# Kernel tuning notes

Measured on AMD Instinct MI355X. Metric: run time of the kernel, lower is better.

## Reference

```python
import jax, jax.numpy as jnp
import numpy as np

D_MODEL = 256
D_INNER = 512      # expand(2) * d_model
D_STATE = 16
DT_RANK = 16       # ceil(256/16)
D_CONV = 4
DEPTH = 2


def _silu(x):
    return x * jax.nn.sigmoid(x)


def _selective_scan(u, dt, A, B, C, D):
    # u,dt: [b,l,d]; A: [d,n]; B,C: [b,l,n]; D: [d]
    dA = jnp.einsum('bld,dn->bldn', dt, A)
    dBu = jnp.einsum('bld,bld,bln->bldn', dt, u, B)
    # torch: F.pad(dA[:,1:], last-l-dim one zero).flip(1).cumsum(1).exp().flip(1)
    dA_shift = jnp.concatenate([dA[:, 1:], jnp.zeros_like(dA[:, :1])], axis=1)
    dAc = jnp.exp(jnp.cumsum(dA_shift[:, ::-1], axis=1)[:, ::-1])
    x = jnp.cumsum(dBu * dAc, axis=1) / (dAc + 1e-12)
    y = jnp.einsum('bldn,bln->bld', x, C)
    return y + u * D


def _block(x, p):
    # x: [b,l,d_model]
    in_w, conv_w, conv_b, xproj_w, dt_w, dt_b, A_log, Dp, out_w = p
    xr = jnp.einsum('bld,ed->ble', x, in_w)           # [b,l,2*d_inner]
    xx, res = jnp.split(xr, 2, axis=-1)
    # causal depthwise conv1d (padding d_conv-1 then truncate == left-pad)
    xc = jax.lax.conv_general_dilated(
        xx.transpose(0, 2, 1), conv_w, window_strides=(1,),
        padding=[(D_CONV - 1, 0)], feature_group_count=D_INNER,
        dimension_numbers=('NCH', 'OIH', 'NCH')) + conv_b[None, :, None]
    xx = _silu(xc.transpose(0, 2, 1))                 # [b,l,d_inner]
    x_dbl = jnp.einsum('bld,ed->ble', xx, xproj_w)
    delta = x_dbl[..., :DT_RANK]
    B = x_dbl[..., DT_RANK:DT_RANK + D_STATE]
    C = x_dbl[..., DT_RANK + D_STATE:]
    delta = jax.nn.softplus(jnp.einsum('blr,dr->bld', delta, dt_w) + dt_b)
    A = -jnp.exp(A_log)
    y = _selective_scan(xx, delta, A, B, C, Dp)
    y = y * _silu(res)
    return jnp.einsum('bld,od->blo', y, out_w)


def _model1(x, params):
    for i in range(DEPTH):
        x = _block(x, tuple(q[i] for q in params))
    return x


def setup_inputs() -> dict:
    key = jax.random.key(0)
    ks = jax.random.split(key, 8)

    def nrm(k, shape, scale):
        return (jax.random.normal(k, shape) * scale).astype(jnp.float32)

    x0 = jax.random.normal(ks[0], (4, D_MODEL, 256, 256), jnp.float32)
    in_w = nrm(ks[1], (DEPTH, 2 * D_INNER, D_MODEL), 0.02)
    conv_w = nrm(ks[2], (DEPTH, D_INNER, 1, D_CONV), 0.1)
    conv_b = jnp.zeros((DEPTH, D_INNER), jnp.float32)
    xproj_w = nrm(ks[3], (DEPTH, DT_RANK + 2 * D_STATE, D_INNER), 0.02)
    dt_w = nrm(ks[4], (DEPTH, D_INNER, DT_RANK), 0.05)
    dt_b = jnp.full((DEPTH, D_INNER), -4.0, jnp.float32)  # small deltas for stability
    A_log = jnp.tile(jnp.log(jnp.arange(1, D_STATE + 1, dtype=jnp.float32))[None, None, :],
                     (DEPTH, D_INNER, 1))
    Dp = jnp.ones((DEPTH, D_INNER), jnp.float32)
    out_w = nrm(ks[5], (DEPTH, D_MODEL, D_INNER), 0.02)
    return dict(x0=x0, in_w=in_w, conv_w=conv_w, conv_b=conv_b, xproj_w=xproj_w,
                dt_w=dt_w, dt_b=dt_b, A_log=A_log, Dp=Dp, out_w=out_w)


def reference(x0, in_w, conv_w, conv_b, xproj_w, dt_w, dt_b, A_log, Dp, out_w):
    params = (in_w, conv_w, conv_b, xproj_w, dt_w, dt_b, A_log, Dp, out_w)
    # h-axis: pool over w, mamba over length h (weights shared with w pass)
    x_h = x0.mean(axis=3)                                        # [b,c,h]
    xm_h = _model1(x_h.transpose(0, 2, 1), params)               # [b,h,c]
    xm_h = xm_h.transpose(0, 2, 1)[..., None] * x0               # [b,c,h,w]
    # w-axis: pool over h of gated map, mamba over length w
    x_w = xm_h.mean(axis=2)                                      # [b,c,w]
    xm_w = _model1(x_w.transpose(0, 2, 1), params)               # [b,w,c]
    return xm_w.transpose(0, 2, 1)[:, :, None, :] * x0           # [b,c,h,w]
```

## Files before the change

### kernel.cpp

```cpp
#include <hip/hip_runtime.h>
#include <math.h>

#define BSZ 4
#define DM 256
#define LL 256
#define DI 512
#define NBL (BSZ * LL)

__device__ __forceinline__ float fast_rcp(float x) { return __builtin_amdgcn_rcpf(x); }
__device__ __forceinline__ float fast_sig(float x) { return fast_rcp(1.0f + __expf(-x)); }

__device__ __forceinline__ void unswz(int j, int& b, int& i) {
    b = (j & 7) >> 1;
    i = ((j >> 3) << 1) | (j & 1);
}

__global__ __launch_bounds__(256) void k_meanw_prep(const float* __restrict__ x0,
                                                    const float* __restrict__ in_w1,
                                                    const float* __restrict__ out_w0,
                                                    float* __restrict__ S0,
                                                    float* __restrict__ Wf) {
    __shared__ float smem[1664];
    int bl = blockIdx.x;
    int tid = threadIdx.x;
    if (bl < 1024) {
        int b, i; unswz(bl, b, i);
        int rowblk = (b << 8) | i;
        int wv = tid >> 6, lane = tid & 63;
        const float4* x4 = (const float4*)x0;
        int rbase = rowblk * 256 + wv * 64;
        for (int i0 = 0; i0 < 64; i0 += 8) {
            float s[8];
#pragma unroll
            for (int j = 0; j < 8; ++j) {
                float4 v = x4[(size_t)(rbase + i0 + j) * 64 + lane];
                s[j] = (v.x + v.y) + (v.z + v.w);
            }
#pragma unroll
            for (int j = 0; j < 8; ++j) {
#pragma unroll
                for (int m = 32; m >= 1; m >>= 1) s[j] += __shfl_xor(s[j], m);
            }
            if (lane == 0) {
#pragma unroll
                for (int j = 0; j < 8; ++j) {
                    int rr = rbase + i0 + j;
                    int bb = rr >> 16, d = (rr >> 8) & 255, h = rr & 255;
                    S0[((size_t)(bb * LL) + h) * DM + d] = s[j] * (1.0f / 256.0f);
                }
            }
        }
    } else {
        float* As = smem;
        float* Bs = smem + 576;
        int t = bl - 1024;
        int e0 = (t >> 4) * 32, k0c = (t & 15) * 32;
        int tx = tid & 15, ty = tid >> 4;
        float acc00 = 0.f, acc01 = 0.f, acc10 = 0.f, acc11 = 0.f;
        for (int dm0 = 0; dm0 < 256; dm0 += 16) {
            float4 v;
            if (tid < 128) {
                int r = tid >> 2, q = tid & 3;
                v = *(const float4*)(in_w1 + (size_t)(e0 + r) * 256 + dm0 + 4 * q);
            } else {
                int idx = tid - 128;
                int r = idx >> 3, q = idx & 7;
                v = *(const float4*)(out_w0 + (size_t)(dm0 + r) * 512 + k0c + 4 * q);
            }
            __syncthreads();
            if (tid < 128) {
                int r = tid >> 2, q = tid & 3;
                As[(4 * q + 0) * 36 + r] = v.x;
                As[(4 * q + 1) * 36 + r] = v.y;
                As[(4 * q + 2) * 36 + r] = v.z;
                As[(4 * q + 3) * 36 + r] = v.w;
            } else {
                int idx = tid - 128;
                int r = idx >> 3, q = idx & 7;
                Bs[r * 36 + 4 * q + 0] = v.x;
                Bs[r * 36 + 4 * q + 1] = v.y;
                Bs[r * 36 + 4 * q + 2] = v.z;
                Bs[r * 36 + 4 * q + 3] = v.w;
            }
            __syncthreads();
#pragma unroll
            for (int kk = 0; kk < 16; ++kk) {
                float2 a = *(const float2*)(As + kk * 36 + 2 * ty);
                float2 b2 = *(const float2*)(Bs + kk * 36 + 2 * tx);
                acc00 = fmaf(a.x, b2.x, acc00);
                acc01 = fmaf(a.x, b2.y, acc01);
                acc10 = fmaf(a.y, b2.x, acc10);
                acc11 = fmaf(a.y, b2.y, acc11);
            }
        }
        float* c0 = Wf + (size_t)(e0 + 2 * ty) * 512 + k0c + 2 * tx;
        c0[0] = acc00; c0[1] = acc01;
        c0[512] = acc10; c0[513] = acc11;
    }
}

__global__ __launch_bounds__(256) void k_gemm_nt64(const float* __restrict__ A,
                                                   const float* __restrict__ Bw,
                                                   float* __restrict__ C) {
    __shared__ float As[16][68];
    __shared__ float Bs[16][68];
    int tid = threadIdx.x;
    int b, i; unswz(blockIdx.x, b, i);
    int m0 = b * 256 + (i >> 4) * 64;
    int n0 = (i & 15) * 64;
    int tx = tid & 15, ty = tid >> 4;
    int r = tid >> 2, kq = (tid & 3) * 4;

    const float* pa = A + (size_t)(m0 + r) * 256 + kq;
    const float* pb = Bw + (size_t)(n0 + r) * 256 + kq;
    float4 ra = *(const float4*)pa;
    float4 rb = *(const float4*)pb;

    float acc[4][4];
#pragma unroll
    for (int ii = 0; ii < 4; ++ii)
#pragma unroll
        for (int jj = 0; jj < 4; ++jj) acc[ii][jj] = 0.0f;

    for (int k0 = 0; k0 < 256; k0 += 16) {
        __syncthreads();
        As[kq + 0][r] = ra.x; As[kq + 1][r] = ra.y; As[kq + 2][r] = ra.z; As[kq + 3][r] = ra.w;
        Bs[kq + 0][r] = rb.x; Bs[kq + 1][r] = rb.y; Bs[kq + 2][r] = rb.z; Bs[kq + 3][r] = rb.w;
        __syncthreads();
        if (k0 + 16 < 256) {
            ra = *(const float4*)(pa + k0 + 16);
            rb = *(const float4*)(pb + k0 + 16);
        }
#pragma unroll
        for (int kk = 0; kk < 16; ++kk) {
            float4 a4 = *(const float4*)(&As[kk][ty * 4]);
            float4 b4 = *(const float4*)(&Bs[kk][tx * 4]);
            float aa[4] = {a4.x, a4.y, a4.z, a4.w};
            float bb[4] = {b4.x, b4.y, b4.z, b4.w};
#pragma unroll
            for (int ii = 0; ii < 4; ++ii)
#pragma unroll
                for (int jj = 0; jj < 4; ++jj)
                    acc[ii][jj] = fmaf(aa[ii], bb[jj], acc[ii][jj]);
        }
    }
#pragma unroll
    for (int ii = 0; ii < 4; ++ii) {
        float4 o;
        o.x = acc[ii][0]; o.y = acc[ii][1]; o.z = acc[ii][2]; o.w = acc[ii][3];
        *(float4*)(C + (size_t)(m0 + ty * 4 + ii) * 1024 + n0 + tx * 4) = o;
    }
}

__global__ __launch_bounds__(256) void k_gemm_tn64(const float* __restrict__ At,
                                                   const float* __restrict__ Bw,
                                                   float* __restrict__ C) {
    __shared__ float As[16][68];
    __shared__ float Bs[16][68];
    int tid = threadIdx.x;
    int b, i; unswz(blockIdx.x, b, i);
    int l0 = (i >> 4) * 64;
    int n0 = (i & 15) * 64;
    int m0 = b * 256 + l0;
    int tx = tid & 15, ty = tid >> 4;
    int rkk = tid >> 4, mq = (tid & 15) * 4;
    int rn = tid >> 2, dq = (tid & 3) * 4;

    const float* pa = At + ((size_t)(b * 512) + rkk) * 256 + l0 + mq;
    const float* pb = Bw + (size_t)(n0 + rn) * 512 + dq;
    float4 ra = *(const float4*)pa;
    float4 rb = *(const float4*)pb;

    float acc[4][4];
#pragma unroll
    for (int ii = 0; ii < 4; ++ii)
#pragma unroll
        for (int jj = 0; jj < 4; ++jj) acc[ii][jj] = 0.0f;

    for (int d0 = 0; d0 < 512; d0 += 16) {
        __syncthreads();
        *(float4*)(&As[rkk][mq]) = ra;
        Bs[dq + 0][rn] = rb.x; Bs[dq + 1][rn] = rb.y; Bs[dq + 2][rn] = rb.z; Bs[dq + 3][rn] = rb.w;
        __syncthreads();
        if (d0 + 16 < 512) {
            ra = *(const float4*)(pa + (size_t)(d0 + 16) * 256);
            rb = *(const float4*)(pb + d0 + 16);
        }
#pragma unroll
        for (int kk = 0; kk < 16; ++kk) {
            float4 a4 = *(const float4*)(&As[kk][ty * 4]);
            float4 b4 = *(const float4*)(&Bs[kk][tx * 4]);
            float aa[4] = {a4.x, a4.y, a4.z, a4.w};
            float bb[4] = {b4.x, b4.y, b4.z, b4.w};
#pragma unroll
            for (int ii = 0; ii < 4; ++ii)
#pragma unroll
                for (int jj = 0; jj < 4; ++jj)
                    acc[ii][jj] = fmaf(aa[ii], bb[jj], acc[ii][jj]);
        }
    }
#pragma unroll
    for (int ii = 0; ii < 4; ++ii) {
        float4 o;
        o.x = acc[ii][0]; o.y = acc[ii][1]; o.z = acc[ii][2]; o.w = acc[ii][3];
        *(float4*)(C + (size_t)(m0 + ty * 4 + ii) * 1024 + n0 + tx * 4) = o;
    }
}

__global__ __launch_bounds__(256) void k_mid(const float* __restrict__ xz,
                                             const float* __restrict__ cw,
                                             const float* __restrict__ cb,
                                             const float* __restrict__ xpw,
                                             float* __restrict__ xx,
                                             float* __restrict__ xdbl) {
    __shared__ float xs[DI];
    __shared__ float pr[256];
    int tid = threadIdx.x;
    int b = (blockIdx.x & 7) >> 1;
    int ib = ((blockIdx.x >> 3) << 1) | (blockIdx.x & 1);

    for (int k = 0; k < 4; ++k) {
        int l = ib + 64 * k;
        int bl = (b << 8) | l;
        __syncthreads();
#pragma unroll
        for (int c = 0; c < 2; ++c) {
            int d = tid + 256 * c;
            float4 w4 = *(const float4*)(cw + d * 4);
            float acc = cb[d];
#pragma unroll
            for (int kk = 0; kk < 4; ++kk) {
                int ls = l + kk - 3;
                float v = (ls >= 0) ? xz[((size_t)(b * LL + ls)) * 1024 + d] : 0.0f;
                acc = fmaf(((const float*)&w4)[kk], v, acc);
            }
            float v = acc * fast_sig(acc);
            xs[d] = v;
            xx[(size_t)bl * DI + d] = v;
        }
        __syncthreads();

        int e = tid >> 2, c2 = tid & 3;
        float a = 0.0f;
        if (e < 48) {
            const float4* xv4 = (const float4*)(xs + c2 * 128);
            const float4* wv4 = (const float4*)(xpw + (size_t)e * DI + c2 * 128);
#pragma unroll 8
            for (int q = 0; q < 32; ++q) {
                float4 x4 = xv4[q], p4 = wv4[q];
                a = fmaf(x4.x, p4.x, a);
                a = fmaf(x4.y, p4.y, a);
                a = fmaf(x4.z, p4.z, a);
                a = fmaf(x4.w, p4.w, a);
            }
        }
        pr[tid] = a;
        __syncthreads();
        if (tid < 48)
            xdbl[(size_t)bl * 48 + tid] = pr[4 * tid] + pr[4 * tid + 1] + pr[4 * tid + 2] + pr[4 * tid + 3];
    }
}

__global__ __launch_bounds__(256) void k_scan(const float* __restrict__ xx,
                                              const float* __restrict__ xdbl,
                                              const float* __restrict__ xz,
                                              const float* __restrict__ Alog,
                                              const float* __restrict__ Dp,
                                              const float* __restrict__ dtw,
                                              const float* __restrict__ dtb,
                                              float* __restrict__ ygT) {
    __shared__ float yred[4][LL];
    __shared__ float us[LL];
    int tid = threadIdx.x;
    int lane = tid & 63, w = tid >> 6;
    int b = (blockIdx.x & 7) >> 1;
    int ib = ((blockIdx.x >> 3) << 1) | (blockIdx.x & 1);
    int l0 = lane * 4;

    for (int kq = 0; kq < 4; ++kq) {
        int d = ib + 128 * kq;
        int seq = b * DI + d;
        __syncthreads();

        const float* xd0 = xdbl + ((size_t)(b * LL) + l0) * 48;
        const float* wr = dtw + d * 16;
        float4 w0 = *(const float4*)(wr + 0);
        float4 w1 = *(const float4*)(wr + 4);
        float4 w2 = *(const float4*)(wr + 8);
        float4 w3 = *(const float4*)(wr + 12);
        float bias = dtb[d];

        float dt[4], u[4], dtu[4], P[4];
#pragma unroll
        for (int i = 0; i < 4; ++i) {
            const float* xr = xd0 + i * 48;
            float4 a0 = *(const float4*)(xr + 0);
            float4 a1 = *(const float4*)(xr + 4);
            float4 a2 = *(const float4*)(xr + 8);
            float4 a3 = *(const float4*)(xr + 12);
            float acc = bias;
            acc = fmaf(a0.x, w0.x, acc); acc = fmaf(a0.y, w0.y, acc);
            acc = fmaf(a0.z, w0.z, acc); acc = fmaf(a0.w, w0.w, acc);
            acc = fmaf(a1.x, w1.x, acc); acc = fmaf(a1.y, w1.y, acc);
            acc = fmaf(a1.z, w1.z, acc); acc = fmaf(a1.w, w1.w, acc);
            acc = fmaf(a2.x, w2.x, acc); acc = fmaf(a2.y, w2.y, acc);
            acc = fmaf(a2.z, w2.z, acc); acc = fmaf(a2.w, w2.w, acc);
            acc = fmaf(a3.x, w3.x, acc); acc = fmaf(a3.y, w3.y, acc);
            acc = fmaf(a3.z, w3.z, acc); acc = fmaf(a3.w, w3.w, acc);
            dt[i] = (acc > 20.0f) ? acc : __logf(1.0f + __expf(acc));
            u[i] = xx[((size_t)(b * LL) + l0 + i) * DI + d];
            dtu[i] = dt[i] * u[i];
        }

        P[0] = dt[0]; P[1] = P[0] + dt[1]; P[2] = P[1] + dt[2]; P[3] = P[2] + dt[3];
        float s = P[3];
#pragma unroll
        for (int off = 1; off < 64; off <<= 1) {
            float t = __shfl_up(s, off);
            if (lane >= off) s += t;
        }
        float base = s - P[3];
        float dt_end = __shfl(s, 63);
        float Dtc[4];
#pragma unroll
        for (int i = 0; i < 4; ++i) Dtc[i] = P[i] + base;

        if (w == 0) {
#pragma unroll
            for (int i = 0; i < 4; ++i) us[l0 + i] = u[i];
        }

        float4 Al = *(const float4*)(Alog + d * 16 + 4 * w);
        float A[4] = {-__expf(Al.x), -__expf(Al.y), -__expf(Al.z), -__expf(Al.w)};
        float Bv[4][4], Cv[4][4];
#pragma unroll
        for (int i = 0; i < 4; ++i) {
            float4 bq = *(const float4*)(xd0 + i * 48 + 16 + 4 * w);
            float4 cq = *(const float4*)(xd0 + i * 48 + 32 + 4 * w);
            Bv[i][0] = bq.x; Bv[i][1] = bq.y; Bv[i][2] = bq.z; Bv[i][3] = bq.w;
            Cv[i][0] = cq.x; Cv[i][1] = cq.y; Cv[i][2] = cq.z; Cv[i][3] = cq.w;
        }

        float y[4] = {0.f, 0.f, 0.f, 0.f};
#pragma unroll
        for (int c = 0; c < 4; ++c) {
            float Ac = A[c];
            float dAc[4], t[4];
#pragma unroll
            for (int i = 0; i < 4; ++i) {
                dAc[i] = __expf(Ac * (dt_end - Dtc[i]));
                t[i] = dtu[i] * Bv[i][c] * dAc[i];
            }
            float p0 = t[0], p1 = p0 + t[1], p2 = p1 + t[2], p3 = p2 + t[3];
            float ss = p3;
#pragma unroll
            for (int off = 1; off < 64; off <<= 1) {
                float tt = __shfl_up(ss, off);
                if (lane >= off) ss += tt;
            }
            float baseT = ss - p3;
            y[0] = fmaf((p0 + baseT) * fast_rcp(dAc[0] + 1e-12f), Cv[0][c], y[0]);
            y[1] = fmaf((p1 + baseT) * fast_rcp(dAc[1] + 1e-12f), Cv[1][c], y[1]);
            y[2] = fmaf((p2 + baseT) * fast_rcp(dAc[2] + 1e-12f), Cv[2][c], y[2]);
            y[3] = fmaf((p3 + baseT) * fast_rcp(dAc[3] + 1e-12f), Cv[3][c], y[3]);
        }
#pragma unroll
        for (int i = 0; i < 4; ++i) yred[w][l0 + i] = y[i];
        __syncthreads();

        int l = tid;
        float ysum = yred[0][l] + yred[1][l] + yred[2][l] + yred[3][l];
        float yv = fmaf(us[l], Dp[d], ysum);
        float res = xz[((size_t)(b * LL) + l) * 1024 + DI + d];
        ygT[(size_t)seq * LL + l] = yv * res * fast_sig(res);
    }
}

__device__ __forceinline__ void outproj_col(const float* __restrict__ ygT,
                                            const float* __restrict__ w1row,
                                            int b, int tid,
                                            float* ws, float* ms) {
    ws[tid] = w1row[tid];
    ws[tid + 256] = w1row[tid + 256];
    __syncthreads();
    const float* yb = ygT + (size_t)(b * 512) * 256 + tid;
    float a0 = 0.f, a1 = 0.f, a2 = 0.f, a3 = 0.f;
#pragma unroll 2
    for (int dd = 0; dd < 512; dd += 8) {
        float v0 = yb[(dd + 0) * 256], v1 = yb[(dd + 1) * 256];
        float v2 = yb[(dd + 2) * 256], v3 = yb[(dd + 3) * 256];
        float v4 = yb[(dd + 4) * 256], v5 = yb[(dd + 5) * 256];
        float v6 = yb[(dd + 6) * 256], v7 = yb[(dd + 7) * 256];
        a0 = fmaf(v0, ws[dd + 0], a0);
        a1 = fmaf(v1, ws[dd + 1], a1);
        a2 = fmaf(v2, ws[dd + 2], a2);
        a3 = fmaf(v3, ws[dd + 3], a3);
        a0 = fmaf(v4, ws[dd + 4], a0);
        a1 = fmaf(v5, ws[dd + 5], a1);
        a2 = fmaf(v6, ws[dd + 6], a2);
        a3 = fmaf(v7, ws[dd + 7], a3);
    }
    ms[tid] = (a0 + a1) + (a2 + a3);
    __syncthreads();
}

__global__ __launch_bounds__(256) void k_outproj_fuse_mean_h(const float* __restrict__ ygT,
                                                             const float* __restrict__ w1,
                                                             const float* __restrict__ x0,
                                                             float* __restrict__ xw) {
    __shared__ float ws[512];
    __shared__ float ms[LL];
    int b, d; unswz(blockIdx.x, b, d);
    int bd = (b << 8) | d;
    int tid = threadIdx.x;
    outproj_col(ygT, w1 + (size_t)d * 512, b, tid, ws, ms);

    int w = tid;
    const float* xrow = x0 + (size_t)bd * 65536;
    float a0 = 0.0f, a1 = 0.0f, a2 = 0.0f, a3 = 0.0f;
    for (int h = 0; h < 256; h += 8) {
        float xv[8];
#pragma unroll
        for (int j = 0; j < 8; ++j) xv[j] = xrow[(size_t)(h + j) * 256 + w];
        a0 = fmaf(ms[h + 0], xv[0], a0);
        a1 = fmaf(ms[h + 1], xv[1], a1);
        a2 = fmaf(ms[h + 2], xv[2], a2);
        a3 = fmaf(ms[h + 3], xv[3], a3);
        a0 = fmaf(ms[h + 4], xv[4], a0);
        a1 = fmaf(ms[h + 5], xv[5], a1);
        a2 = fmaf(ms[h + 6], xv[6], a2);
        a3 = fmaf(ms[h + 7], xv[7], a3);
    }
    float acc = (a0 + a1) + (a2 + a3);
    xw[((size_t)(b * LL) + w) * DM + d] = acc * (1.0f / 256.0f);
}

__global__ __launch_bounds__(256) void k_outproj_final(const float* __restrict__ ygT,
                                                       const float* __restrict__ w1,
                                                       const float* __restrict__ x0,
                                                       float* __restrict__ out) {
    __shared__ float ws[512];
    __shared__ float ms[LL];
    int b, d; unswz(blockIdx.x, b, d);
    int bd = (b << 8) | d;
    int tid = threadIdx.x;
    outproj_col(ygT, w1 + (size_t)d * 512, b, tid, ws, ms);

    int w4 = tid & 63;
    int hq = tid >> 6;
    float4 mv = *(const float4*)(ms + (w4 << 2));
    const float4* xin = (const float4*)(x0 + (size_t)bd * 65536);
    float4* oout = (float4*)(out + (size_t)bd * 65536);
#pragma unroll 4
    for (int hi = 0; hi < 64; ++hi) {
        int h = hi * 4 + hq;
        size_t idx = (size_t)h * 64 + w4;
        float4 xv = xin[idx];
        float4 o;
        o.x = mv.x * xv.x;
        o.y = mv.y * xv.y;
        o.z = mv.z * xv.z;
        o.w = mv.w * xv.w;
        oout[idx] = o;
    }
}

extern "C" void kernel_launch(void* const* d_in, const int* in_sizes, int n_in,
                              void* d_out, int out_size, void* d_ws, size_t ws_size,
                              hipStream_t stream) {
    const float* x0      = (const float*)d_in[0];
    const float* in_w    = (const float*)d_in[1];
    const float* conv_w  = (const float*)d_in[2];
    const float* conv_b  = (const float*)d_in[3];
    const float* xproj_w = (const float*)d_in[4];
    const float* dt_w    = (const float*)d_in[5];
    const float* dt_b    = (const float*)d_in[6];
    const float* A_log   = (const float*)d_in[7];
    const float* Dp      = (const float*)d_in[8];
    const float* out_w   = (const float*)d_in[9];
    float* out = (float*)d_out;

    float* S0   = (float*)d_ws;
    float* Wf   = S0 + 262144;
    float* xz   = Wf + 524288;
    float* xx   = xz + 1048576;
    float* xdbl = xx + 524288;
    float* ygT  = xdbl + 49152;

    const float* out_w1 = out_w + 131072;

    auto run_model_core = [&](const float* inb) {
        k_gemm_nt64<<<256, 256, 0, stream>>>(inb, in_w, xz);
        k_mid<<<256, 256, 0, stream>>>(xz, conv_w, conv_b, xproj_w, xx, xdbl);
        k_scan<<<512, 256, 0, stream>>>(xx, xdbl, xz, A_log, Dp, dt_w, dt_b, ygT);
        k_gemm_tn64<<<256, 256, 0, stream>>>(ygT, Wf, xz);
        k_mid<<<256, 256, 0, stream>>>(xz, conv_w + 2048, conv_b + 512,
                                       xproj_w + 24576, xx, xdbl);
        k_scan<<<512, 256, 0, stream>>>(xx, xdbl, xz, A_log + 8192, Dp + 512,
                                        dt_w + 8192, dt_b + 512, ygT);
    };

    k_meanw_prep<<<1536, 256, 0, stream>>>(x0, in_w + 262144, out_w, S0, Wf);
    run_model_core(S0);
    k_outproj_fuse_mean_h<<<NBL, 256, 0, stream>>>(ygT, out_w1, x0, S0);
    run_model_core(S0);
    k_outproj_final<<<NBL, 256, 0, stream>>>(ygT, out_w1, x0, out);
}
```

Baseline: 472.7 us.

## Store pooled inputs transposed and recompute causal conv in scan

```diff
diff --git a/kernel.cpp b/kernel.cpp
--- a/kernel.cpp
+++ b/kernel.cpp
@@ -18,14 +18,14 @@
 __global__ __launch_bounds__(256) void k_meanw_prep(const float* __restrict__ x0,
                                                     const float* __restrict__ in_w1,
                                                     const float* __restrict__ out_w0,
-                                                    float* __restrict__ S0,
+                                                    float* __restrict__ S0T,
                                                     float* __restrict__ Wf) {
     __shared__ float smem[1664];
     int bl = blockIdx.x;
     int tid = threadIdx.x;
     if (bl < 1024) {
-        int b, i; unswz(bl, b, i);
-        int rowblk = (b << 8) | i;
+        int b, dch; unswz(bl, b, dch);
+        int rowblk = (b << 8) | dch;
         int wv = tid >> 6, lane = tid & 63;
         const float4* x4 = (const float4*)x0;
         int rbase = rowblk * 256 + wv * 64;
@@ -42,12 +42,13 @@
                 for (int m = 32; m >= 1; m >>= 1) s[j] += __shfl_xor(s[j], m);
             }
             if (lane == 0) {
-#pragma unroll
-                for (int j = 0; j < 8; ++j) {
-                    int rr = rbase + i0 + j;
-                    int bb = rr >> 16, d = (rr >> 8) & 255, h = rr & 255;
-                    S0[((size_t)(bb * LL) + h) * DM + d] = s[j] * (1.0f / 256.0f);
-                }
+                float4 o1, o2;
+                o1.x = s[0] * (1.0f / 256.0f); o1.y = s[1] * (1.0f / 256.0f);
+                o1.z = s[2] * (1.0f / 256.0f); o1.w = s[3] * (1.0f / 256.0f);
+                o2.x = s[4] * (1.0f / 256.0f); o2.y = s[5] * (1.0f / 256.0f);
+                o2.z = s[6] * (1.0f / 256.0f); o2.w = s[7] * (1.0f / 256.0f);
+                *(float4*)(S0T + (size_t)rbase + i0) = o1;
+                *(float4*)(S0T + (size_t)rbase + i0 + 4) = o2;
             }
         }
     } else {
@@ -99,62 +100,9 @@
     }
 }
 
-__global__ __launch_bounds__(256) void k_gemm_nt64(const float* __restrict__ A,
-                                                   const float* __restrict__ Bw,
-                                                   float* __restrict__ C) {
-    __shared__ float As[16][68];
-    __shared__ float Bs[16][68];
-    int tid = threadIdx.x;
-    int b, i; unswz(blockIdx.x, b, i);
-    int m0 = b * 256 + (i >> 4) * 64;
-    int n0 = (i & 15) * 64;
-    int tx = tid & 15, ty = tid >> 4;
-    int r = tid >> 2, kq = (tid & 3) * 4;
-
-    const float* pa = A + (size_t)(m0 + r) * 256 + kq;
-    const float* pb = Bw + (size_t)(n0 + r) * 256 + kq;
-    float4 ra = *(const float4*)pa;
-    float4 rb = *(const float4*)pb;
-
-    float acc[4][4];
-#pragma unroll
-    for (int ii = 0; ii < 4; ++ii)
-#pragma unroll
-        for (int jj = 0; jj < 4; ++jj) acc[ii][jj] = 0.0f;
-
-    for (int k0 = 0; k0 < 256; k0 += 16) {
-        __syncthreads();
-        As[kq + 0][r] = ra.x; As[kq + 1][r] = ra.y; As[kq + 2][r] = ra.z; As[kq + 3][r] = ra.w;
-        Bs[kq + 0][r] = rb.x; Bs[kq + 1][r] = rb.y; Bs[kq + 2][r] = rb.z; Bs[kq + 3][r] = rb.w;
-        __syncthreads();
-        if (k0 + 16 < 256) {
-            ra = *(const float4*)(pa + k0 + 16);
-            rb = *(const float4*)(pb + k0 + 16);
-        }
-#pragma unroll
-        for (int kk = 0; kk < 16; ++kk) {
-            float4 a4 = *(const float4*)(&As[kk][ty * 4]);
-            float4 b4 = *(const float4*)(&Bs[kk][tx * 4]);
-            float aa[4] = {a4.x, a4.y, a4.z, a4.w};
-            float bb[4] = {b4.x, b4.y, b4.z, b4.w};
-#pragma unroll
-            for (int ii = 0; ii < 4; ++ii)
-#pragma unroll
-                for (int jj = 0; jj < 4; ++jj)
-                    acc[ii][jj] = fmaf(aa[ii], bb[jj], acc[ii][jj]);
-        }
-    }
-#pragma unroll
-    for (int ii = 0; ii < 4; ++ii) {
-        float4 o;
-        o.x = acc[ii][0]; o.y = acc[ii][1]; o.z = acc[ii][2]; o.w = acc[ii][3];
-        *(float4*)(C + (size_t)(m0 + ty * 4 + ii) * 1024 + n0 + tx * 4) = o;
-    }
-}
-
-__global__ __launch_bounds__(256) void k_gemm_tn64(const float* __restrict__ At,
-                                                   const float* __restrict__ Bw,
-                                                   float* __restrict__ C) {
+__global__ __launch_bounds__(256) void k_gemm_tn_inproj(const float* __restrict__ S0T,
+                                                        const float* __restrict__ Bw,
+                                                        float* __restrict__ C) {
     __shared__ float As[16][68];
     __shared__ float Bs[16][68];
     int tid = threadIdx.x;
@@ -166,8 +114,8 @@
     int rkk = tid >> 4, mq = (tid & 15) * 4;
     int rn = tid >> 2, dq = (tid & 3) * 4;
 
-    const float* pa = At + ((size_t)(b * 512) + rkk) * 256 + l0 + mq;
-    const float* pb = Bw + (size_t)(n0 + rn) * 512 + dq;
+    const float* pa = S0T + ((size_t)(b * 256) + rkk) * 256 + l0 + mq;
+    const float* pb = Bw + (size_t)(n0 + rn) * 256 + dq;
     float4 ra = *(const float4*)pa;
     float4 rb = *(const float4*)pb;
 
@@ -177,12 +125,12 @@
 #pragma unroll
         for (int jj = 0; jj < 4; ++jj) acc[ii][jj] = 0.0f;
 
-    for (int d0 = 0; d0 < 512; d0 += 16) {
+    for (int d0 = 0; d0 < 256; d0 += 16) {
         __syncthreads();
         *(float4*)(&As[rkk][mq]) = ra;
         Bs[dq + 0][rn] = rb.x; Bs[dq + 1][rn] = rb.y; Bs[dq + 2][rn] = rb.z; Bs[dq + 3][rn] = rb.w;
         __syncthreads();
-        if (d0 + 16 < 512) {
+        if (d0 + 16 < 256) {
             ra = *(const float4*)(pa + (size_t)(d0 + 16) * 256);
             rb = *(const float4*)(pb + d0 + 16);
         }
@@ -207,11 +155,65 @@
     }
 }
 
+__global__ __launch_bounds__(256) void k_gemm_tn64(const float* __restrict__ At,
+                                                   const float* __restrict__ Bw,
+                                                   float* __restrict__ C) {
+    __shared__ float As[16][68];
+    __shared__ float Bs[16][68];
+    int tid = threadIdx.x;
+    int b, i; unswz(blockIdx.x, b, i);
+    int l0 = (i >> 4) * 64;
+    int n0 = (i & 15) * 64;
+    int m0 = b * 256 + l0;
+    int tx = tid & 15, ty = tid >> 4;
+    int rkk = tid >> 4, mq = (tid & 15) * 4;
+    int rn = tid >> 2, dq = (tid & 3) * 4;
+
+    const float* pa = At + ((size_t)(b * 512) + rkk) * 256 + l0 + mq;
+    const float* pb = Bw + (size_t)(n0 + rn) * 512 + dq;
+    float4 ra = *(const float4*)pa;
+    float4 rb = *(const float4*)pb;
+
+    float acc[4][4];
+#pragma unroll
+    for (int ii = 0; ii < 4; ++ii)
+#pragma unroll
+        for (int jj = 0; jj < 4; ++jj) acc[ii][jj] = 0.0f;
+
+    for (int d0 = 0; d0 < 512; d0 += 16) {
+        __syncthreads();
+        *(float4*)(&As[rkk][mq]) = ra;
+        Bs[dq + 0][rn] = rb.x; Bs[dq + 1][rn] = rb.y; Bs[dq + 2][rn] = rb.z; Bs[dq + 3][rn] = rb.w;
+        __syncthreads();
+        if (d0 + 16 < 512) {
+            ra = *(const float4*)(pa + (size_t)(d0 + 16) * 256);
+            rb = *(const float4*)(pb + d0 + 16);
+        }
+#pragma unroll
+        for (int kk = 0; kk < 16; ++kk) {
+            float4 a4 = *(const float4*)(&As[kk][ty * 4]);
+            float4 b4 = *(const float4*)(&Bs[kk][tx * 4]);
+            float aa[4] = {a4.x, a4.y, a4.z, a4.w};
+            float bb[4] = {b4.x, b4.y, b4.z, b4.w};
+#pragma unroll
+            for (int ii = 0; ii < 4; ++ii)
+#pragma unroll
+                for (int jj = 0; jj < 4; ++jj)
+                    acc[ii][jj] = fmaf(aa[ii], bb[jj], acc[ii][jj]);
+        }
+    }
+#pragma unroll
+    for (int ii = 0; ii < 4; ++ii) {
+        float4 o;
+        o.x = acc[ii][0]; o.y = acc[ii][1]; o.z = acc[ii][2]; o.w = acc[ii][3];
+        *(float4*)(C + (size_t)(m0 + ty * 4 + ii) * 1024 + n0 + tx * 4) = o;
+    }
+}
+
 __global__ __launch_bounds__(256) void k_mid(const float* __restrict__ xz,
                                              const float* __restrict__ cw,
                                              const float* __restrict__ cb,
                                              const float* __restrict__ xpw,
-                                             float* __restrict__ xx,
                                              float* __restrict__ xdbl) {
     __shared__ float xs[DI];
     __shared__ float pr[256];
@@ -234,9 +236,7 @@
                 float v = (ls >= 0) ? xz[((size_t)(b * LL + ls)) * 1024 + d] : 0.0f;
                 acc = fmaf(((const float*)&w4)[kk], v, acc);
             }
-            float v = acc * fast_sig(acc);
-            xs[d] = v;
-            xx[(size_t)bl * DI + d] = v;
+            xs[d] = acc * fast_sig(acc);
         }
         __syncthreads();
 
@@ -261,9 +261,10 @@
     }
 }
 
-__global__ __launch_bounds__(256) void k_scan(const float* __restrict__ xx,
-                                              const float* __restrict__ xdbl,
+__global__ __launch_bounds__(256) void k_scan(const float* __restrict__ xdbl,
                                               const float* __restrict__ xz,
+                                              const float* __restrict__ cw,
+                                              const float* __restrict__ cb,
                                               const float* __restrict__ Alog,
                                               const float* __restrict__ Dp,
                                               const float* __restrict__ dtw,
@@ -289,6 +290,8 @@
         float4 w2 = *(const float4*)(wr + 8);
         float4 w3 = *(const float4*)(wr + 12);
         float bias = dtb[d];
+        float4 w4c = *(const float4*)(cw + d * 4);
+        float cbias = cb[d];
 
         float dt[4], u[4], dtu[4], P[4];
 #pragma unroll
@@ -308,7 +311,14 @@
             acc = fmaf(a3.x, w3.x, acc); acc = fmaf(a3.y, w3.y, acc);
             acc = fmaf(a3.z, w3.z, acc); acc = fmaf(a3.w, w3.w, acc);
             dt[i] = (acc > 20.0f) ? acc : __logf(1.0f + __expf(acc));
-            u[i] = xx[((size_t)(b * LL) + l0 + i) * DI + d];
+            float ua = cbias;
+#pragma unroll
+            for (int kk = 0; kk < 4; ++kk) {
+                int ls = l0 + i + kk - 3;
+                float v = (ls >= 0) ? xz[((size_t)(b * LL + ls)) * 1024 + d] : 0.0f;
+                ua = fmaf(((const float*)&w4c)[kk], v, ua);
+            }
+            u[i] = ua * fast_sig(ua);
             dtu[i] = dt[i] * u[i];
         }
 
@@ -407,7 +417,7 @@
 __global__ __launch_bounds__(256) void k_outproj_fuse_mean_h(const float* __restrict__ ygT,
                                                              const float* __restrict__ w1,
                                                              const float* __restrict__ x0,
-                                                             float* __restrict__ xw) {
+                                                             float* __restrict__ S0T) {
     __shared__ float ws[512];
     __shared__ float ms[LL];
     int b, d; unswz(blockIdx.x, b, d);
@@ -432,7 +442,7 @@
         a3 = fmaf(ms[h + 7], xv[7], a3);
     }
     float acc = (a0 + a1) + (a2 + a3);
-    xw[((size_t)(b * LL) + w) * DM + d] = acc * (1.0f / 256.0f);
+    S0T[(size_t)bd * 256 + w] = acc * (1.0f / 256.0f);
 }
 
 __global__ __launch_bounds__(256) void k_outproj_final(const float* __restrict__ ygT,
@@ -480,29 +490,30 @@
     const float* out_w   = (const float*)d_in[9];
     float* out = (float*)d_out;
 
-    float* S0   = (float*)d_ws;
-    float* Wf   = S0 + 262144;
+    float* S0T  = (float*)d_ws;
+    float* Wf   = S0T + 262144;
     float* xz   = Wf + 524288;
-    float* xx   = xz + 1048576;
-    float* xdbl = xx + 524288;
+    float* xdbl = xz + 1048576;
     float* ygT  = xdbl + 49152;
 
     const float* out_w1 = out_w + 131072;
 
-    auto run_model_core = [&](const float* inb) {
-        k_gemm_nt64<<<256, 256, 0, stream>>>(inb, in_w, xz);
-        k_mid<<<256, 256, 0, stream>>>(xz, conv_w, conv_b, xproj_w, xx, xdbl);
-        k_scan<<<512, 256, 0, stream>>>(xx, xdbl, xz, A_log, Dp, dt_w, dt_b, ygT);
+    auto run_model_core = [&]() {
+        k_gemm_tn_inproj<<<256, 256, 0, stream>>>(S0T, in_w, xz);
+        k_mid<<<256, 256, 0, stream>>>(xz, conv_w, conv_b, xproj_w, xdbl);
+        k_scan<<<512, 256, 0, stream>>>(xdbl, xz, conv_w, conv_b,
+                                        A_log, Dp, dt_w, dt_b, ygT);
         k_gemm_tn64<<<256, 256, 0, stream>>>(ygT, Wf, xz);
         k_mid<<<256, 256, 0, stream>>>(xz, conv_w + 2048, conv_b + 512,
-                                       xproj_w + 24576, xx, xdbl);
-        k_scan<<<512, 256, 0, stream>>>(xx, xdbl, xz, A_log + 8192, Dp + 512,
+                                       xproj_w + 24576, xdbl);
+        k_scan<<<512, 256, 0, stream>>>(xdbl, xz, conv_w + 2048, conv_b + 512,
+                                        A_log + 8192, Dp + 512,
                                         dt_w + 8192, dt_b + 512, ygT);
     };
 
-    k_meanw_prep<<<1536, 256, 0, stream>>>(x0, in_w + 262144, out_w, S0, Wf);
-    run_model_core(S0);
-    k_outproj_fuse_mean_h<<<NBL, 256, 0, stream>>>(ygT, out_w1, x0, S0);
-    run_model_core(S0);
+    k_meanw_prep<<<1536, 256, 0, stream>>>(x0, in_w + 262144, out_w, S0T, Wf);
+    run_model_core();
+    k_outproj_fuse_mean_h<<<NBL, 256, 0, stream>>>(ygT, out_w1, x0, S0T);
+    run_model_core();
     k_outproj_final<<<NBL, 256, 0, stream>>>(ygT, out_w1, x0, out);
 }
```

New measurement: 481.0 us. Within noise of the previous version (+1.8%).
